# Performance work log

Hardware: AMD Instinct MI355X
Metric: run time of the kernel (lower is better)

The kernel has to match this reference:

```python
import jax, jax.numpy as jnp
from jax import lax
import numpy as np

B, N, CIN, COUT, HID = 16, 4096, 64, 128, 128
RATIO, K = 0.25, 32
M = int(N * RATIO)  # 1024 sampled centroids per cloud


def setup_inputs() -> dict:
    key = jax.random.key(0)
    ks = jax.random.split(key, 6)
    s = 0.02
    return {
        "x": jax.random.normal(ks[0], (B, N, CIN), jnp.float32),
        "pos": jax.random.normal(ks[1], (B, N, 3), jnp.float32),
        "W1": jax.random.normal(ks[2], (CIN + 3, HID), jnp.float32) * s,
        "b1": jnp.zeros((HID,), jnp.float32),
        "W2": jax.random.normal(ks[3], (HID, COUT), jnp.float32) * s,
        "b2": jnp.zeros((COUT,), jnp.float32),
        "Wlin": jax.random.normal(ks[4], (CIN, COUT), jnp.float32) * s,
        "blin": jnp.zeros((COUT,), jnp.float32),
    }


def mish(v):
    return v * jnp.tanh(jax.nn.softplus(v))


def fps(pc, m):
    # Farthest point sampling (deterministic start at index 0, as PyG with random_start=False).
    n = pc.shape[0]

    def step(carry, _):
        mind, last = carry
        d = jnp.sum((pc - pc[last]) ** 2, axis=-1)  # [N]
        mind = jnp.minimum(mind, d)
        nxt = jnp.argmax(mind).astype(jnp.int32)
        return (mind, nxt), nxt

    init = (jnp.full((n,), np.inf, pc.dtype), jnp.int32(0))
    _, rest = lax.scan(step, init, None, length=m - 1)
    return jnp.concatenate([jnp.zeros((1,), jnp.int32), rest])  # [M]


def reference(x, pos, W1, b1, W2, b2, Wlin, blin):
    def per_cloud(xc, pc):
        # xc: [N,CIN], pc: [N,3]
        idx = fps(pc, M)                                        # [M]
        q = pc[idx]                                             # [M,3] sampled centroids
        d2 = jnp.sum((q[:, None, :] - pc[None, :, :]) ** 2, -1)  # [M,N]
        _, nbr = lax.top_k(-d2, K)                              # [M,K] knn indices
        rel = pc[nbr] - q[:, None, :]                           # [M,K,3]
        h = jnp.concatenate([xc[nbr], rel], axis=-1)            # [M,K,CIN+3]
        h = mish(h @ W1 + b1)                                   # local_nn layer 1
        h = h @ W2 + b2                                         # [M,K,COUT]
        agg = jnp.max(h, axis=1)                                # PointNetConv max aggregation
        out = agg + xc[idx] @ Wlin + blin                       # residual skip via self.lin
        return out, q

    x_out, pos_out = jax.vmap(per_cloud)(x, pos)
    return x_out, pos_out
```

## Files before the change

### kernel.cpp

```cpp
#include <hip/hip_runtime.h>
#include <hip/hip_bf16.h>

constexpr int B    = 16;
constexpr int N    = 4096;
constexpr int CIN  = 64;
constexpr int COUT = 128;
constexpr int M    = 1024;
constexpr int K    = 32;

constexpr int K1  = 96;
constexpr int LDH = 136;

typedef __attribute__((ext_vector_type(8))) short short8;
typedef __attribute__((ext_vector_type(4))) short short4v;
typedef __attribute__((ext_vector_type(4))) float f32x4;
typedef __attribute__((ext_vector_type(2))) float f32x2;

static __device__ __forceinline__ unsigned short f2bf(float f) {
  unsigned u = __float_as_uint(f);
  unsigned r = (u + 0x7FFFu + ((u >> 16) & 1u)) >> 16;
  return (unsigned short)r;
}

static __device__ __forceinline__ float fast_mish(float v) {
  float u = __expf(v);
  float s = u * (u + 2.0f);
  float den = s + 2.0f;
  float r;
  asm("v_rcp_f32 %0, %1" : "=v"(r) : "v"(den));
  float t = s * r;
  return (v > 60.f) ? v : v * t;
}

template <int CTRL, int RM>
static __device__ __forceinline__ unsigned dpp_umax_step(unsigned x) {
  int o = __builtin_amdgcn_update_dpp((int)x, (int)x, CTRL, RM, 0xF, false);
  unsigned u = (unsigned)o;
  return x > u ? x : u;
}
static __device__ __forceinline__ unsigned wave_umax(unsigned x) {
  x = dpp_umax_step<0x111, 0xF>(x);
  x = dpp_umax_step<0x112, 0xF>(x);
  x = dpp_umax_step<0x114, 0xF>(x);
  x = dpp_umax_step<0x118, 0xF>(x);
  x = dpp_umax_step<0x142, 0xA>(x);
  x = dpp_umax_step<0x143, 0xC>(x);
  return (unsigned)__builtin_amdgcn_readlane((int)x, 63);
}

static __device__ __forceinline__ unsigned long long umax64(unsigned long long a,
                                                            unsigned long long b) {
  return a > b ? a : b;
}

__global__ __launch_bounds__(512) void fps8_kernel(const float* __restrict__ pos,
                                                   int* __restrict__ idx_out,
                                                   float* __restrict__ pout,
                                                   float* __restrict__ pos4) {
#pragma clang fp contract(off)
  const int b   = blockIdx.x;
  const int tid = threadIdx.x;
  __shared__ float sp[N][4];
  __shared__ unsigned long long skey[2][8];
  const float* p = pos + (size_t)b * (N * 3);
  float* p4 = pos4 + (size_t)b * N * 4;

  f32x2 px2[4], py2[4], pz2[4];
  float mind[8];
#pragma unroll
  for (int j = 0; j < 8; j++) {
    const int n = tid + j * 512;
    const float x = p[3 * n + 0];
    const float y = p[3 * n + 1];
    const float z = p[3 * n + 2];
    px2[j >> 1][j & 1] = x;
    py2[j >> 1][j & 1] = y;
    pz2[j >> 1][j & 1] = z;
    mind[j] = __builtin_inff();
    f32x4 v;
    v[0] = x; v[1] = y; v[2] = z; v[3] = 0.f;
    *(f32x4*)(&sp[n][0]) = v;
    *(f32x4*)(p4 + 4 * n) = v;
  }
  float qx = p[0], qy = p[1], qz = p[2];
  if (tid == 0) {
    idx_out[b * M + 0] = 0;
    pout[(size_t)(b * M + 0) * 3 + 0] = qx;
    pout[(size_t)(b * M + 0) * 3 + 1] = qy;
    pout[(size_t)(b * M + 0) * 3 + 2] = qz;
  }
  __syncthreads();

  const int wv = tid >> 6, lane = tid & 63;
  for (int t = 1; t < M; t++) {
    const f32x2 nqx = {-qx, -qx};
    const f32x2 nqy = {-qy, -qy};
    const f32x2 nqz = {-qz, -qz};
    float bv = -1.f;
    unsigned bn = 0;
#pragma unroll
    for (int k = 0; k < 4; k++) {
      f32x2 dx = px2[k] + nqx;
      f32x2 dy = py2[k] + nqy;
      f32x2 dz = pz2[k] + nqz;
      f32x2 s = (dx * dx + dy * dy) + dz * dz;
      const float mi0 = fminf(mind[2 * k + 0], s.x);
      mind[2 * k + 0] = mi0;
      bool c0 = mi0 > bv;
      bv = c0 ? mi0 : bv;
      bn = c0 ? (unsigned)(tid + (2 * k + 0) * 512) : bn;
      const float mi1 = fminf(mind[2 * k + 1], s.y);
      mind[2 * k + 1] = mi1;
      bool c1 = mi1 > bv;
      bv = c1 ? mi1 : bv;
      bn = c1 ? (unsigned)(tid + (2 * k + 1) * 512) : bn;
    }
    const unsigned vb = __float_as_uint(bv);
    const unsigned wb = wave_umax(vb);
    unsigned tk = (vb == wb) ? ~bn : 0u;
    tk = wave_umax(tk);
    const int par = t & 1;
    if (lane == 0) skey[par][wv] = ((unsigned long long)wb << 32) | tk;
    __syncthreads();
    const unsigned long long k0 = skey[par][0];
    const unsigned long long k1 = skey[par][1];
    const unsigned long long k2 = skey[par][2];
    const unsigned long long k3 = skey[par][3];
    const unsigned long long k4 = skey[par][4];
    const unsigned long long k5 = skey[par][5];
    const unsigned long long k6 = skey[par][6];
    const unsigned long long k7 = skey[par][7];
    const unsigned long long bb =
        umax64(umax64(umax64(k0, k1), umax64(k2, k3)),
               umax64(umax64(k4, k5), umax64(k6, k7)));
    const unsigned n = ~(unsigned)bb;
    const f32x4 qv = *(const f32x4*)(&sp[n][0]);
    qx = qv[0];
    qy = qv[1];
    qz = qv[2];
    if (tid == 0) {
      idx_out[b * M + t] = (int)n;
      pout[(size_t)(b * M + t) * 3 + 0] = qx;
      pout[(size_t)(b * M + t) * 3 + 1] = qy;
      pout[(size_t)(b * M + t) * 3 + 2] = qz;
    }
  }
}

__global__ __launch_bounds__(256) void prep_weights(const float* __restrict__ W1,
                                                    const float* __restrict__ W2,
                                                    unsigned short* __restrict__ W1t,
                                                    unsigned short* __restrict__ W2t) {
  const int n = blockIdx.x;
  const int t = threadIdx.x;
  if (t < K1) {
    W1t[n * K1 + t] = (t < 67) ? f2bf(W1[t * 128 + n]) : (unsigned short)0;
  } else if (t < K1 + 128) {
    int k = t - K1;
    W2t[n * 128 + k] = f2bf(W2[k * 128 + n]);
  }
}

__global__ __launch_bounds__(512) void knn6_kernel(const float* __restrict__ pos4,
                                                   const int* __restrict__ idx,
                                                   int* __restrict__ nbr) {
#pragma clang fp contract(off)
  __shared__ float sp4[N * 4];
  const int tid  = threadIdx.x;
  const int wv   = tid >> 6;
  const int lane = tid & 63;
  const int cent = blockIdx.x * 8 + wv;
  const int b = cent >> 10;
  const float* p4 = pos4 + (size_t)b * N * 4;
  for (int i = tid; i < N; i += 512) {
    *(f32x4*)(sp4 + 4 * i) = *(const f32x4*)(p4 + 4 * i);
  }
  __syncthreads();

  const int sel = idx[cent];
  const f32x4 q = *(const f32x4*)(sp4 + 4 * sel);
  const f32x2 nqx = {-q[0], -q[0]};
  const f32x2 nqy = {-q[1], -q[1]};
  const f32x2 nqz = {-q[2], -q[2]};

  float d[64];
#pragma unroll
  for (int jj = 0; jj < 32; jj++) {
    const f32x4 v0 = *(const f32x4*)(sp4 + 4 * ((2 * jj + 0) * 64 + lane));
    const f32x4 v1 = *(const f32x4*)(sp4 + 4 * ((2 * jj + 1) * 64 + lane));
    f32x2 vx = {v0[0], v1[0]};
    f32x2 vy = {v0[1], v1[1]};
    f32x2 vz = {v0[2], v1[2]};
    f32x2 dx = vx + nqx;
    f32x2 dy = vy + nqy;
    f32x2 dz = vz + nqz;
    f32x2 s = (dx * dx + dy * dy) + dz * dz;
    d[2 * jj + 0] = s.x;
    d[2 * jj + 1] = s.y;
  }
  float gv[8];
  int gj[8];
#pragma unroll
  for (int g = 0; g < 8; g++) {
    gv[g] = __builtin_inff();
    gj[g] = 8 * g;
#pragma unroll
    for (int e = 0; e < 8; e++) {
      const int j = 8 * g + e;
      bool c = d[j] < gv[g];
      gv[g] = c ? d[j] : gv[g];
      gj[g] = c ? j : gj[g];
    }
  }

  int* out = nbr + (size_t)cent * K;
  for (int r = 0; r < K; r++) {
    float bv = __builtin_inff();
    int bj = 0;
#pragma unroll
    for (int g = 0; g < 8; g++) {
      bool c = gv[g] < bv;
      bv = c ? gv[g] : bv;
      bj = c ? gj[g] : bj;
    }
    const unsigned bn = (unsigned)(bj * 64 + lane);
    const unsigned nb = ~__float_as_uint(bv);
    const unsigned wnb = wave_umax(nb);
    unsigned tk = (nb == wnb) ? (0xFFFFFFFFu - bn) : 0u;
    tk = wave_umax(tk);
    const unsigned wn = 0xFFFFFFFFu - tk;
    if (lane == 0) out[r] = (int)wn;

    const int wj = (int)(wn >> 6);
    const int wl = (int)(wn & 63);
    const int wg = wj >> 3;
#pragma unroll
    for (int g = 0; g < 8; g++) {
      if (g == wg) {
#pragma unroll
        for (int e = 0; e < 8; e++) {
          if (8 * g + e == wj) {
            if (lane == wl) d[8 * g + e] = __builtin_inff();
          }
        }
        float nv = __builtin_inff();
        int nj = 8 * g;
#pragma unroll
        for (int e = 0; e < 8; e++) {
          const int j = 8 * g + e;
          bool c = d[j] < nv;
          nv = c ? d[j] : nv;
          nj = c ? j : nj;
        }
        gv[g] = nv;
        gj[g] = nj;
      }
    }
  }
}

__global__ __launch_bounds__(256) void mlp4_kernel(
    const float* __restrict__ x, const float* __restrict__ pos4,
    const unsigned short* __restrict__ W1t, const unsigned short* __restrict__ W2t,
    const float* __restrict__ b1, const float* __restrict__ b2,
    const float* __restrict__ Wlin, const float* __restrict__ blin,
    const int* __restrict__ idx, const int* __restrict__ nbr,
    float* __restrict__ xout) {
  __shared__ unsigned short sA2[4][32][LDH];
  const int tid  = threadIdx.x;
  const int wv   = tid >> 6;
  const int lane = tid & 63;
  const int lrow = lane & 15;
  const int g    = lane >> 4;
  unsigned short* A2 = &sA2[wv][0][0];
  const int cent = blockIdx.x * 4 + wv;
  const int b    = cent >> 10;
  const int sel  = idx[cent];
  const float* p4 = pos4 + (size_t)b * N * 4;
  const f32x4 q = *(const f32x4*)(p4 + 4 * sel);
  const float qx = q[0], qy = q[1], qz = q[2];

  const int n0 = nbr[(size_t)cent * K + lrow];
  const int n1 = nbr[(size_t)cent * K + 16 + lrow];

  short8 a0[3], a1[3];
  {
    const float* xr0 = x + ((size_t)b * N + n0) * CIN;
    const float* xr1 = x + ((size_t)b * N + n1) * CIN;
#pragma unroll
    for (int kc = 0; kc < 2; kc++) {
      const int k0 = kc * 32 + g * 8;
      f32x4 u0 = *(const f32x4*)(xr0 + k0);
      f32x4 u1 = *(const f32x4*)(xr0 + k0 + 4);
      f32x4 v0 = *(const f32x4*)(xr1 + k0);
      f32x4 v1 = *(const f32x4*)(xr1 + k0 + 4);
      short8 ha, hb;
#pragma unroll
      for (int e = 0; e < 4; e++) {
        ha[e] = (short)f2bf(u0[e]);
        ha[e + 4] = (short)f2bf(u1[e]);
        hb[e] = (short)f2bf(v0[e]);
        hb[e + 4] = (short)f2bf(v1[e]);
      }
      a0[kc] = ha;
      a1[kc] = hb;
    }
    short8 z = {};
    a0[2] = z;
    a1[2] = z;
    if (g == 0) {
      float r0x = p4[4 * n0 + 0] - qx, r0y = p4[4 * n0 + 1] - qy, r0z = p4[4 * n0 + 2] - qz;
      float r1x = p4[4 * n1 + 0] - qx, r1y = p4[4 * n1 + 1] - qy, r1z = p4[4 * n1 + 2] - qz;
      a0[2][0] = (short)f2bf(r0x); a0[2][1] = (short)f2bf(r0y); a0[2][2] = (short)f2bf(r0z);
      a1[2][0] = (short)f2bf(r1x); a1[2][1] = (short)f2bf(r1y); a1[2][2] = (short)f2bf(r1z);
    }
  }

#pragma unroll 2
  for (int nt = 0; nt < 8; nt++) {
    const unsigned short* w1r = W1t + (size_t)(nt * 16 + lrow) * K1 + g * 8;
    f32x4 c0 = {}, c1 = {};
#pragma unroll
    for (int kc = 0; kc < 3; kc++) {
      short8 afr = *(const short8*)(w1r + kc * 32);
      c0 = __builtin_amdgcn_mfma_f32_16x16x32_bf16(afr, a0[kc], c0, 0, 0, 0);
      c1 = __builtin_amdgcn_mfma_f32_16x16x32_bf16(afr, a1[kc], c1, 0, 0, 0);
    }
    const int kbase = nt * 16 + g * 4;
    const f32x4 bb = *(const f32x4*)(b1 + kbase);
    short4v h0, h1;
#pragma unroll
    for (int reg = 0; reg < 4; reg++) {
      h0[reg] = (short)f2bf(fast_mish(c0[reg] + bb[reg]));
      h1[reg] = (short)f2bf(fast_mish(c1[reg] + bb[reg]));
    }
    *(short4v*)(A2 + lrow * LDH + kbase) = h0;
    *(short4v*)(A2 + (16 + lrow) * LDH + kbase) = h1;
  }

  f32x4 xq[4];
  {
    const float* xs = x + ((size_t)b * N + sel) * CIN + g * 16;
#pragma unroll
    for (int v = 0; v < 4; v++) xq[v] = *(const f32x4*)(xs + 4 * v);
  }

#pragma unroll 2
  for (int nt = 0; nt < 8; nt++) {
    const unsigned short* w2r = W2t + (size_t)(nt * 16 + lrow) * 128 + g * 8;
    f32x4 c0 = {}, c1 = {};
#pragma unroll
    for (int kc = 0; kc < 4; kc++) {
      short8 af0 = *(const short8*)(A2 + lrow * LDH + kc * 32 + g * 8);
      short8 af1 = *(const short8*)(A2 + (16 + lrow) * LDH + kc * 32 + g * 8);
      short8 bfr = *(const short8*)(w2r + kc * 32);
      c0 = __builtin_amdgcn_mfma_f32_16x16x32_bf16(af0, bfr, c0, 0, 0, 0);
      c1 = __builtin_amdgcn_mfma_f32_16x16x32_bf16(af1, bfr, c1, 0, 0, 0);
    }
    float pm = fmaxf(fmaxf(fmaxf(c0[0], c0[1]), fmaxf(c0[2], c0[3])),
                     fmaxf(fmaxf(c1[0], c1[1]), fmaxf(c1[2], c1[3])));
    pm = fmaxf(pm, __shfl_xor(pm, 16, 64));
    pm = fmaxf(pm, __shfl_xor(pm, 32, 64));
    const int j = nt * 16 + lrow;
    float s = 0.f;
#pragma unroll
    for (int e = 0; e < 16; e++) {
      s += xq[e >> 2][e & 3] * Wlin[(g * 16 + e) * 128 + j];
    }
    s += __shfl_xor(s, 16, 64);
    s += __shfl_xor(s, 32, 64);
    if (g == 0) {
      xout[(size_t)cent * 128 + j] = pm + b2[j] + s + blin[j];
    }
  }
}

extern "C" void kernel_launch(void* const* d_in, const int* in_sizes, int n_in,
                              void* d_out, int out_size, void* d_ws, size_t ws_size,
                              hipStream_t stream) {
  const float* x    = (const float*)d_in[0];
  const float* pos  = (const float*)d_in[1];
  const float* W1   = (const float*)d_in[2];
  const float* b1   = (const float*)d_in[3];
  const float* W2   = (const float*)d_in[4];
  const float* b2   = (const float*)d_in[5];
  const float* Wlin = (const float*)d_in[6];
  const float* blin = (const float*)d_in[7];

  float* out  = (float*)d_out;
  float* xout = out;
  float* pout = out + (size_t)B * M * COUT;

  char* ws = (char*)d_ws;
  int* idx            = (int*)ws;
  int* nbr            = (int*)(ws + 65536);
  unsigned short* W1t = (unsigned short*)(ws + 65536 + 2097152);
  unsigned short* W2t = (unsigned short*)(ws + 65536 + 2097152 + 24576);
  float* pos4         = (float*)(ws + 65536 + 2097152 + 24576 + 32768);

  prep_weights<<<dim3(128), dim3(256), 0, stream>>>(W1, W2, W1t, W2t);
  fps8_kernel<<<dim3(B), dim3(512), 0, stream>>>(pos, idx, pout, pos4);
  knn6_kernel<<<dim3(B * M / 8), dim3(512), 0, stream>>>(pos4, idx, nbr);
  mlp4_kernel<<<dim3(B * M / 4), dim3(256), 0, stream>>>(
      x, pos4, W1t, W2t, b1, b2, Wlin, blin, idx, nbr, xout);
}
```

Measured before the change: 935.8 us.

## Widen FPS to 1024 threads and fold weight prep into knn launch

The FPS kernel now runs with 1024 threads per cloud, so each thread holds 4 points instead of 8, and the per-thread argmax is computed after the min update with a max-then-equality index selection. The cross-wave reduction grows to 16 keys. The weight-transpose kernel is folded into extra blocks of the knn launch, removing one kernel launch. Because FPS is a 1023-step serial loop with a block barrier each step, the shorter per-thread work may be offset by the costlier barrier and reduction across 16 waves.

```diff
diff --git a/kernel.cpp b/kernel.cpp
--- a/kernel.cpp
+++ b/kernel.cpp
@@ -10,6 +10,7 @@
 
 constexpr int K1  = 96;
 constexpr int LDH = 136;
+constexpr int KNN_BLOCKS = B * M / 8;
 
 typedef __attribute__((ext_vector_type(8))) short short8;
 typedef __attribute__((ext_vector_type(4))) short short4v;
@@ -53,23 +54,23 @@
   return a > b ? a : b;
 }
 
-__global__ __launch_bounds__(512) void fps8_kernel(const float* __restrict__ pos,
-                                                   int* __restrict__ idx_out,
-                                                   float* __restrict__ pout,
-                                                   float* __restrict__ pos4) {
+__global__ __launch_bounds__(1024) void fps9_kernel(const float* __restrict__ pos,
+                                                    int* __restrict__ idx_out,
+                                                    float* __restrict__ pout,
+                                                    float* __restrict__ pos4) {
 #pragma clang fp contract(off)
   const int b   = blockIdx.x;
   const int tid = threadIdx.x;
   __shared__ float sp[N][4];
-  __shared__ unsigned long long skey[2][8];
+  __shared__ unsigned long long skey[2][16];
   const float* p = pos + (size_t)b * (N * 3);
   float* p4 = pos4 + (size_t)b * N * 4;
 
-  f32x2 px2[4], py2[4], pz2[4];
-  float mind[8];
-#pragma unroll
-  for (int j = 0; j < 8; j++) {
-    const int n = tid + j * 512;
+  f32x2 px2[2], py2[2], pz2[2];
+  float mind[4];
+#pragma unroll
+  for (int j = 0; j < 4; j++) {
+    const int n = tid + j * 1024;
     const float x = p[3 * n + 0];
     const float y = p[3 * n + 1];
     const float z = p[3 * n + 2];
@@ -96,25 +97,21 @@
     const f32x2 nqx = {-qx, -qx};
     const f32x2 nqy = {-qy, -qy};
     const f32x2 nqz = {-qz, -qz};
-    float bv = -1.f;
-    unsigned bn = 0;
-#pragma unroll
-    for (int k = 0; k < 4; k++) {
+#pragma unroll
+    for (int k = 0; k < 2; k++) {
       f32x2 dx = px2[k] + nqx;
       f32x2 dy = py2[k] + nqy;
       f32x2 dz = pz2[k] + nqz;
       f32x2 s = (dx * dx + dy * dy) + dz * dz;
-      const float mi0 = fminf(mind[2 * k + 0], s.x);
-      mind[2 * k + 0] = mi0;
-      bool c0 = mi0 > bv;
-      bv = c0 ? mi0 : bv;
-      bn = c0 ? (unsigned)(tid + (2 * k + 0) * 512) : bn;
-      const float mi1 = fminf(mind[2 * k + 1], s.y);
-      mind[2 * k + 1] = mi1;
-      bool c1 = mi1 > bv;
-      bv = c1 ? mi1 : bv;
-      bn = c1 ? (unsigned)(tid + (2 * k + 1) * 512) : bn;
-    }
+      mind[2 * k + 0] = fminf(mind[2 * k + 0], s.x);
+      mind[2 * k + 1] = fminf(mind[2 * k + 1], s.y);
+    }
+    const float bv = fmaxf(fmaxf(mind[0], mind[1]), fmaxf(mind[2], mind[3]));
+    unsigned bn = (unsigned)(tid + 3 * 1024);
+    bn = (mind[2] == bv) ? (unsigned)(tid + 2 * 1024) : bn;
+    bn = (mind[1] == bv) ? (unsigned)(tid + 1 * 1024) : bn;
+    bn = (mind[0] == bv) ? (unsigned)tid : bn;
+
     const unsigned vb = __float_as_uint(bv);
     const unsigned wb = wave_umax(vb);
     unsigned tk = (vb == wb) ? ~bn : 0u;
@@ -122,17 +119,17 @@
     const int par = t & 1;
     if (lane == 0) skey[par][wv] = ((unsigned long long)wb << 32) | tk;
     __syncthreads();
-    const unsigned long long k0 = skey[par][0];
-    const unsigned long long k1 = skey[par][1];
-    const unsigned long long k2 = skey[par][2];
-    const unsigned long long k3 = skey[par][3];
-    const unsigned long long k4 = skey[par][4];
-    const unsigned long long k5 = skey[par][5];
-    const unsigned long long k6 = skey[par][6];
-    const unsigned long long k7 = skey[par][7];
+    unsigned long long m0 = umax64(skey[par][0], skey[par][1]);
+    unsigned long long m1 = umax64(skey[par][2], skey[par][3]);
+    unsigned long long m2 = umax64(skey[par][4], skey[par][5]);
+    unsigned long long m3 = umax64(skey[par][6], skey[par][7]);
+    unsigned long long m4 = umax64(skey[par][8], skey[par][9]);
+    unsigned long long m5 = umax64(skey[par][10], skey[par][11]);
+    unsigned long long m6 = umax64(skey[par][12], skey[par][13]);
+    unsigned long long m7 = umax64(skey[par][14], skey[par][15]);
     const unsigned long long bb =
-        umax64(umax64(umax64(k0, k1), umax64(k2, k3)),
-               umax64(umax64(k4, k5), umax64(k6, k7)));
+        umax64(umax64(umax64(m0, m1), umax64(m2, m3)),
+               umax64(umax64(m4, m5), umax64(m6, m7)));
     const unsigned n = ~(unsigned)bb;
     const f32x4 qv = *(const f32x4*)(&sp[n][0]);
     qx = qv[0];
@@ -147,25 +144,26 @@
   }
 }
 
-__global__ __launch_bounds__(256) void prep_weights(const float* __restrict__ W1,
-                                                    const float* __restrict__ W2,
-                                                    unsigned short* __restrict__ W1t,
-                                                    unsigned short* __restrict__ W2t) {
-  const int n = blockIdx.x;
-  const int t = threadIdx.x;
-  if (t < K1) {
-    W1t[n * K1 + t] = (t < 67) ? f2bf(W1[t * 128 + n]) : (unsigned short)0;
-  } else if (t < K1 + 128) {
-    int k = t - K1;
-    W2t[n * 128 + k] = f2bf(W2[k * 128 + n]);
-  }
-}
-
 __global__ __launch_bounds__(512) void knn6_kernel(const float* __restrict__ pos4,
                                                    const int* __restrict__ idx,
-                                                   int* __restrict__ nbr) {
+                                                   int* __restrict__ nbr,
+                                                   const float* __restrict__ W1,
+                                                   const float* __restrict__ W2,
+                                                   unsigned short* __restrict__ W1t,
+                                                   unsigned short* __restrict__ W2t) {
 #pragma clang fp contract(off)
   __shared__ float sp4[N * 4];
+  if (blockIdx.x >= KNN_BLOCKS) {
+    const int n = blockIdx.x - KNN_BLOCKS;
+    const int t = threadIdx.x;
+    if (t < K1) {
+      W1t[n * K1 + t] = (t < 67) ? f2bf(W1[t * 128 + n]) : (unsigned short)0;
+    } else if (t < K1 + 128) {
+      const int k = t - K1;
+      W2t[n * 128 + k] = f2bf(W2[k * 128 + n]);
+    }
+    return;
+  }
   const int tid  = threadIdx.x;
   const int wv   = tid >> 6;
   const int lane = tid & 63;
@@ -398,9 +396,9 @@
   unsigned short* W2t = (unsigned short*)(ws + 65536 + 2097152 + 24576);
   float* pos4         = (float*)(ws + 65536 + 2097152 + 24576 + 32768);
 
-  prep_weights<<<dim3(128), dim3(256), 0, stream>>>(W1, W2, W1t, W2t);
-  fps8_kernel<<<dim3(B), dim3(512), 0, stream>>>(pos, idx, pout, pos4);
-  knn6_kernel<<<dim3(B * M / 8), dim3(512), 0, stream>>>(pos4, idx, nbr);
+  fps9_kernel<<<dim3(B), dim3(1024), 0, stream>>>(pos, idx, pout, pos4);
+  knn6_kernel<<<dim3(KNN_BLOCKS + 128), dim3(512), 0, stream>>>(
+      pos4, idx, nbr, W1, W2, W1t, W2t);
   mlp4_kernel<<<dim3(B * M / 4), dim3(256), 0, stream>>>(
       x, pos4, W1t, W2t, b1, b2, Wlin, blin, idx, nbr, xout);
 }
```

New measurement: 1.198 ms. +28.1%, slower.
